# Kernel tuning notes

Measured on AMD Instinct MI355X. Metric: run time of the kernel, lower is better.

Reference implementation:

```python
import jax, jax.numpy as jnp
import numpy as np

# Config matching init_kwargs / input shapes
DIM = 96        # dim == C
NH = 6          # num_heads
KS = 7          # kernel_size (local window)
GW = 4          # group_width for the grouped conv in Hadamard-attn branch
B, D, H, W = 2, 8, 96, 96
HD = DIM // NH          # head dim (dim_qk == dim_v == dim)
SCALE = HD ** -0.5      # qk_scale default: head_dim**-0.5
PAD = KS // 2
EPS = 1e-5


def setup_inputs() -> dict:
    key = jax.random.key(0)
    ks = jax.random.split(key, 10)
    s = 0.02
    return {
        "x": jax.random.normal(ks[0], (B, DIM, D, H, W), jnp.float32),
        # pre-norm LayerNorm params
        "ln_g": jnp.ones((DIM,), jnp.float32),
        "ln_b": jnp.zeros((DIM,), jnp.float32),
        # q,k projection (fused 1x1): out = 2*dim_qk
        "w_qk": s * jax.random.normal(ks[1], (2 * DIM, DIM), jnp.float32),
        "b_qk": jnp.zeros((2 * DIM,), jnp.float32),
        # v projection (1x1)
        "w_v": s * jax.random.normal(ks[2], (DIM, DIM), jnp.float32),
        "b_v": jnp.zeros((DIM,), jnp.float32),
        # Hadamard-attention branch: grouped KSxKS conv (groups = DIM//GW)
        "w_a1": s * jax.random.normal(ks[3], (DIM, GW, KS, KS), jnp.float32),
        "b_a1": jnp.zeros((DIM,), jnp.float32),
        # 1x1 conv producing per-head local attention logits (NH * KS^2 channels)
        "w_a2": s * jax.random.normal(ks[4], (NH * KS * KS, DIM), jnp.float32),
        "b_a2": jnp.zeros((NH * KS * KS,), jnp.float32),
        # ghost head (lam=1, gamma=1): attn = h_attn * ghost_mul + ghost_add
        "g_mul": 1.0 + s * jax.random.normal(ks[5], (NH * KS * KS,), jnp.float32),
        "g_add": s * jax.random.normal(ks[6], (NH * KS * KS,), jnp.float32),
        # output projection (1x1)
        "w_p": s * jax.random.normal(ks[7], (DIM, DIM), jnp.float32),
        "b_p": jnp.zeros((DIM,), jnp.float32),
    }


def _elsa_block(x, ln_g, ln_b, w_qk, b_qk, w_v, b_v, w_a1, b_a1, w_a2, b_a2,
                g_mul, g_add, w_p, b_p):
    """x: (Bp, H, W, C) channel-last frames. Pre-norm residual ELSA attention."""
    Bp, Hh, Ww, C = x.shape
    # LayerNorm over channels
    mu = jnp.mean(x, axis=-1, keepdims=True)
    var = jnp.mean(jnp.square(x - mu), axis=-1, keepdims=True)
    xn = (x - mu) * jax.lax.rsqrt(var + EPS) * ln_g + ln_b

    # 1x1 q,k,v projections (channel-last matmuls)
    qk = xn @ w_qk.T + b_qk                      # (Bp,H,W,2C)
    q, k = jnp.split(qk, 2, axis=-1)
    v = xn @ w_v.T + b_v                         # (Bp,H,W,C)

    # Hadamard product -> attention logits via grouped conv + GELU + 1x1
    h = jnp.transpose(q * k * SCALE, (0, 3, 1, 2))   # (Bp,C,H,W) NCHW
    a = jax.lax.conv_general_dilated(
        h, w_a1, window_strides=(1, 1), padding='SAME',
        feature_group_count=C // GW) + b_a1[None, :, None, None]
    a = jax.nn.gelu(a, approximate=False)
    a = jnp.einsum('bchw,oc->bohw', a, w_a2) + b_a2[None, :, None, None]

    # ghost head (lam=1, gamma=1): elementwise scale + static bias per (head, tap)
    attn = a * g_mul[None, :, None, None] + g_add[None, :, None, None]
    attn = attn.reshape(Bp, NH, KS * KS, Hh, Ww)     # (Bp,nh,k^2,H,W)

    # local window aggregation (unfold-free: 49 shifted fused multiply-adds)
    vr = jnp.transpose(v, (0, 3, 1, 2)).reshape(Bp, NH, HD, Hh, Ww)
    vp = jnp.pad(vr, ((0, 0), (0, 0), (0, 0), (PAD, PAD), (PAD, PAD)))
    out = jnp.zeros_like(vr)
    for i in range(KS):
        for j in range(KS):
            out = out + attn[:, :, i * KS + j, None] * vp[:, :, :, i:i + Hh, j:j + Ww]

    out = jnp.transpose(out.reshape(Bp, C, Hh, Ww), (0, 2, 3, 1))  # (Bp,H,W,C)
    y = out @ w_p.T + b_p
    return x + y


def reference(x, ln_g, ln_b, w_qk, b_qk, w_v, b_v, w_a1, b_a1, w_a2, b_a2,
              g_mul, g_add, w_p, b_p):
    b, c, d, hh, ww = x.shape
    # 'b c s h w -> (b s) h w c'
    xf = jnp.transpose(x, (0, 2, 3, 4, 1)).reshape(b * d, hh, ww, c)
    yf = _elsa_block(xf, ln_g, ln_b, w_qk, b_qk, w_v, b_v, w_a1, b_a1,
                     w_a2, b_a2, g_mul, g_add, w_p, b_p)
    # '(b s) h w c -> b c s h w'
    return jnp.transpose(yf.reshape(b, d, hh, ww, c), (0, 4, 1, 2, 3))
```

## Files before the change

kernel.cpp:

```cpp
#include <hip/hip_runtime.h>
#include <hip/hip_bf16.h>


typedef unsigned short u16;
typedef short bf16x8 __attribute__((ext_vector_type(8)));
typedef float floatx4 __attribute__((ext_vector_type(4)));
typedef unsigned short ushort8 __attribute__((ext_vector_type(8)));
typedef unsigned int uint4v __attribute__((ext_vector_type(4)));
typedef unsigned int uint2v __attribute__((ext_vector_type(2)));
typedef _Float16 f16x2 __attribute__((ext_vector_type(2)));

#define PIX      9216
#define SCALE_QK 0.25f

__device__ __forceinline__ float lo2f(unsigned int u) {
  union { unsigned int i; float f; } z; z.i = u << 16; return z.f;
}
__device__ __forceinline__ float hi2f(unsigned int u) {
  union { unsigned int i; float f; } z; z.i = u & 0xFFFF0000u; return z.f;
}
__device__ __forceinline__ u16 f2b(float f) {
  union { float f; unsigned int i; } z; z.f = f;
  unsigned int r = z.i + 0x7fffu + ((z.i >> 16) & 1u);
  return (u16)(r >> 16);
}
__device__ __forceinline__ u16 f2h(float f) {
  _Float16 h = (_Float16)f;
  union { _Float16 h; u16 u; } z; z.h = h; return z.u;
}
__device__ __forceinline__ f16x2 upk(unsigned int u) {
  union { unsigned int u; f16x2 h; } z; z.u = u; return z.h;
}
__device__ __forceinline__ f16x2 pkfma(unsigned int w, unsigned int x, f16x2 c) {
#if __has_builtin(__builtin_elementwise_fma)
  return __builtin_elementwise_fma(upk(w), upk(x), c);
#else
  return upk(w) * upk(x) + c;
#endif
}

__global__ void k_prep(const float* __restrict__ w_qk, const float* __restrict__ b_qk,
                       const float* __restrict__ w_v,  const float* __restrict__ b_v,
                       const float* __restrict__ w_a1,
                       const float* __restrict__ w_a2, const float* __restrict__ b_a2,
                       const float* __restrict__ g_mul,const float* __restrict__ g_add,
                       const float* __restrict__ w_p,  const float* __restrict__ b_p,
                       u16* __restrict__ W2, float* __restrict__ bias2,
                       u16* __restrict__ WA2, float* __restrict__ biasA2,
                       u16* __restrict__ WP, float* __restrict__ biasP,
                       unsigned int* __restrict__ WCV) {
  int i = blockIdx.x * 256 + threadIdx.x;
  if (i < 30720) {
    int r = i / 96, ci = i % 96;
    float val = 0.f;
    if (r < 192) { int src = (r & 1) ? (96 + (r >> 1)) : (r >> 1); val = w_qk[src * 96 + ci]; }
    else if (r < 288) val = w_v[(r - 192) * 96 + ci];
    W2[i] = f2b(val);
  } else if (i < 31040) {
    int r = i - 30720; float bv = 0.f;
    if (r < 192) { int src = (r & 1) ? (96 + (r >> 1)) : (r >> 1); bv = b_qk[src]; }
    else if (r < 288) bv = b_v[r - 192];
    bias2[r] = bv;
  } else if (i < 61760) {
    int j = i - 31040; int r = j / 96, ci = j % 96;
    float wv = 0.f;
    if (r < 294) wv = w_a2[r * 96 + ci] * g_mul[r];
    WA2[j] = f2b(wv);
  } else if (i < 62080) {
    int r = i - 61760; float bv = 0.f;
    if (r < 294) bv = b_a2[r] * g_mul[r] + g_add[r];
    biasA2[r] = bv;
  } else if (i < 74368) {
    int j = i - 62080; int r = j / 96;
    WP[j] = (r < 96) ? f2b(w_p[j]) : (u16)0;
  } else if (i < 74496) {
    int r = i - 74368;
    biasP[r] = (r < 96) ? b_p[r] : 0.f;
  } else if (i < 93312) {
    int j = i - 74496;
    int kx = j % 7, co = (j / 7) & 3, ky = (j / 28) % 7, ch = (j / 196) & 3, g = j / 784;
    float w = w_a1[(g * 4 + co) * 196 + ch * 49 + ky * 7 + kx];
    unsigned int hw = f2h(w);
    WCV[j] = hw | (hw << 16);
  }
}

template <int MODE>
__global__ __launch_bounds__(256) void k_gemm(const u16* __restrict__ X,
                                              const u16* __restrict__ W,
                                              const float* __restrict__ bias,
                                              u16* __restrict__ out0,
                                              u16* __restrict__ out1,
                                              float* __restrict__ outF,
                                              const float* __restrict__ resid,
                                              const float* __restrict__ lg,
                                              const float* __restrict__ lb,
                                              int fArg) {
  constexpr int NC = (MODE == 2) ? 2 : 5;
  __shared__ u16 lw[64 * 104];
  __shared__ u16 lx[64 * 104];
  const int tid = threadIdx.x;
  const int fc = blockIdx.y;
  const int f = (MODE == 1) ? (fArg + fc) : fc;
  const int p0 = blockIdx.x * 64;

  if constexpr (MODE == 0) {
    const int pix = tid >> 2, sub = tid & 3;
    const int b = f >> 3, d = f & 7;
    const size_t xbase = ((size_t)(b * 768 + d)) * PIX + p0 + pix;
    float xv[24];
    #pragma unroll
    for (int k = 0; k < 24; ++k)
      xv[k] = resid[xbase + (size_t)(sub * 24 + k) * 73728];
    float s = 0.f, ss = 0.f;
    #pragma unroll
    for (int k = 0; k < 24; ++k) { s += xv[k]; ss += xv[k] * xv[k]; }
    s += __shfl_xor(s, 1);  ss += __shfl_xor(ss, 1);
    s += __shfl_xor(s, 2);  ss += __shfl_xor(ss, 2);
    float mu = s * (1.f / 96.f);
    float var = ss * (1.f / 96.f) - mu * mu;
    float rs = rsqrtf(var + 1e-5f);
    unsigned int* dst = (unsigned int*)&lx[pix * 104 + sub * 24];
    #pragma unroll
    for (int k = 0; k < 12; ++k) {
      int c = sub * 24 + 2 * k;
      u16 lo = f2b((xv[2 * k]     - mu) * rs * lg[c]     + lb[c]);
      u16 hi = f2b((xv[2 * k + 1] - mu) * rs * lg[c + 1] + lb[c + 1]);
      dst[k] = (unsigned int)lo | ((unsigned int)hi << 16);
    }
  } else {
    for (int idx = tid; idx < 768; idx += 256) {
      int s2 = idx >> 6, r = idx & 63;
      const u16* src0 = &X[((size_t)(f * 24 + 2 * s2) * PIX + p0 + r) * 4];
      const u16* src1 = &X[((size_t)(f * 24 + 2 * s2 + 1) * PIX + p0 + r) * 4];
      *(uint2v*)&lx[r * 104 + s2 * 8]     = *(const uint2v*)src0;
      *(uint2v*)&lx[r * 104 + s2 * 8 + 4] = *(const uint2v*)src1;
    }
  }
  __syncthreads();

  const int lane = tid & 63, wv = tid >> 6;
  const int cw = (wv >> 1) * 32, pw = (wv & 1) * 32;
  const int m = lane & 15, quad = lane >> 4;

  for (int cot = 0; cot < NC; ++cot) {
    for (int ch = tid; ch < 768; ch += 256) {
      int r = ch / 12, s2 = ch % 12;
      *(uint4v*)&lw[r * 104 + s2 * 8] =
          *(const uint4v*)&W[(size_t)(cot * 64 + r) * 96 + s2 * 8];
    }
    __syncthreads();

    floatx4 acc[2][2] = {};
    for (int ks = 0; ks < 3; ++ks) {
      int ko = ks * 32 + quad * 8;
      bf16x8 a0 = *(const bf16x8*)&lw[(cw + m) * 104 + ko];
      bf16x8 a1 = *(const bf16x8*)&lw[(cw + 16 + m) * 104 + ko];
      bf16x8 b0 = *(const bf16x8*)&lx[(pw + m) * 104 + ko];
      bf16x8 b1 = *(const bf16x8*)&lx[(pw + 16 + m) * 104 + ko];
      acc[0][0] = __builtin_amdgcn_mfma_f32_16x16x32_bf16(a0, b0, acc[0][0], 0, 0, 0);
      acc[0][1] = __builtin_amdgcn_mfma_f32_16x16x32_bf16(a0, b1, acc[0][1], 0, 0, 0);
      acc[1][0] = __builtin_amdgcn_mfma_f32_16x16x32_bf16(a1, b0, acc[1][0], 0, 0, 0);
      acc[1][1] = __builtin_amdgcn_mfma_f32_16x16x32_bf16(a1, b1, acc[1][1], 0, 0, 0);
    }

    for (int mt = 0; mt < 2; ++mt)
      for (int nt = 0; nt < 2; ++nt) {
        int R = cot * 64 + cw + mt * 16 + quad * 4;
        int pc = p0 + pw + nt * 16 + m;
        floatx4 v4 = acc[mt][nt];
        if (MODE == 0) {
          if (cot < 3) {
            float q0 = v4[0] + bias[R + 0], k0 = v4[1] + bias[R + 1];
            float q1 = v4[2] + bias[R + 2], k1 = v4[3] + bias[R + 3];
            int hc = R >> 1;
            out0[((size_t)f * 96 + hc) * PIX + pc]     = f2h(q0 * k0 * SCALE_QK);
            out0[((size_t)f * 96 + hc + 1) * PIX + pc] = f2h(q1 * k1 * SCALE_QK);
          } else {
            for (int r = 0; r < 4; ++r) {
              int vr = R + r - 192;
              if (vr < 96) out1[((size_t)f * 96 + vr) * PIX + pc] = f2b(v4[r] + bias[R + r]);
            }
          }
        } else if (MODE == 1) {
          for (int r = 0; r < 4; ++r) {
            int o = R + r;
            if (o < 294) out0[((size_t)fc * 294 + o) * PIX + pc] = f2b(v4[r] + bias[o]);
          }
        } else {
          int b = f >> 3, dd = f & 7;
          for (int r = 0; r < 4; ++r) {
            int o = R + r;
            if (o < 96) {
              size_t gi = ((size_t)(b * 96 + o) * 8 + dd) * PIX + pc;
              outF[gi] = resid[gi] + v4[r] + bias[o];
            }
          }
        }
      }
    __syncthreads();
  }
}

__global__ __launch_bounds__(256, 4) void k_conv(const u16* __restrict__ h,
                                                 const unsigned int* __restrict__ wcv,
                                                 const float* __restrict__ b_a1,
                                                 u16* __restrict__ a_t) {
  __shared__ u16 li[4 * 22 * 104];
  const int g = blockIdx.x, ty = blockIdx.y, f = blockIdx.z;
  const int tid = threadIdx.x;
  const int gb = g * 4, y0 = ty * 16;
  for (int idx = tid; idx < 4576; idx += 256) {
    int row = idx / 52;
    int jd  = idx - row * 52;
    int ch  = row / 22;
    int rr  = row - ch * 22;
    int ay  = y0 - 3 + rr;
    unsigned int val = 0;
    if (jd >= 2 && jd <= 49 && ay >= 0 && ay < 96)
      val = *(const unsigned int*)&h[((size_t)f * 96 + gb + ch) * PIX + ay * 96 + (2 * jd - 4)];
    *(unsigned int*)&li[row * 104 + 2 * jd] = val;
  }
  __syncthreads();

  const int y = tid >> 4;
  const int x0 = (tid & 15) * 6;
  f16x2 pacc[4][3];
  #pragma unroll
  for (int co = 0; co < 4; ++co)
    #pragma unroll
    for (int p = 0; p < 3; ++p) pacc[co][p] = upk(0u);

  for (int ch = 0; ch < 4; ++ch) {
    const unsigned int* wch = &wcv[784 * g + 196 * ch];
    for (int ky = 0; ky < 7; ++ky) {
      const unsigned int* lsrc =
          (const unsigned int*)&li[(ch * 22 + (y + ky)) * 104 + x0];
      unsigned int D0 = lsrc[0], D1 = lsrc[1], D2 = lsrc[2], D3 = lsrc[3];
      unsigned int D4 = lsrc[4], D5 = lsrc[5], D6 = lsrc[6];
      unsigned int S0 = __builtin_amdgcn_alignbit(D1, D0, 16);
      unsigned int S1 = __builtin_amdgcn_alignbit(D2, D1, 16);
      unsigned int S2 = __builtin_amdgcn_alignbit(D3, D2, 16);
      unsigned int S3 = __builtin_amdgcn_alignbit(D4, D3, 16);
      unsigned int S4 = __builtin_amdgcn_alignbit(D5, D4, 16);
      unsigned int S5 = __builtin_amdgcn_alignbit(D6, D5, 16);
      const unsigned int* wb = wch + 28 * ky;
      #pragma unroll
      for (int co = 0; co < 4; ++co) {
        unsigned int w0 = wb[co * 7 + 0], w1 = wb[co * 7 + 1];
        unsigned int w2 = wb[co * 7 + 2], w3 = wb[co * 7 + 3];
        unsigned int w4 = wb[co * 7 + 4], w5 = wb[co * 7 + 5];
        unsigned int w6 = wb[co * 7 + 6];
        f16x2 a;
        a = pacc[co][0];
        a = pkfma(w0, S0, a); a = pkfma(w1, D1, a); a = pkfma(w2, S1, a);
        a = pkfma(w3, D2, a); a = pkfma(w4, S2, a); a = pkfma(w5, D3, a);
        a = pkfma(w6, S3, a); pacc[co][0] = a;
        a = pacc[co][1];
        a = pkfma(w0, S1, a); a = pkfma(w1, D2, a); a = pkfma(w2, S2, a);
        a = pkfma(w3, D3, a); a = pkfma(w4, S3, a); a = pkfma(w5, D4, a);
        a = pkfma(w6, S4, a); pacc[co][1] = a;
        a = pacc[co][2];
        a = pkfma(w0, S2, a); a = pkfma(w1, D3, a); a = pkfma(w2, S3, a);
        a = pkfma(w3, D4, a); a = pkfma(w4, S4, a); a = pkfma(w5, D5, a);
        a = pkfma(w6, S5, a); pacc[co][2] = a;
      }
    }
  }

  size_t obase = ((size_t)(f * 24 + g) * PIX + (size_t)(y0 + y) * 96 + x0) * 4;
  float bv0 = b_a1[gb + 0], bv1 = b_a1[gb + 1], bv2 = b_a1[gb + 2], bv3 = b_a1[gb + 3];
  #pragma unroll
  for (int p = 0; p < 3; ++p) {
    ushort8 r8;
    #pragma unroll
    for (int co = 0; co < 4; ++co) {
      float bv = (co == 0) ? bv0 : (co == 1) ? bv1 : (co == 2) ? bv2 : bv3;
      f16x2 v = pacc[co][p];
      float a0 = (float)v[0] + bv, a1 = (float)v[1] + bv;
      r8[co]     = f2b(0.5f * a0 * (1.f + erff(a0 * 0.70710678118f)));
      r8[co + 4] = f2b(0.5f * a1 * (1.f + erff(a1 * 0.70710678118f)));
    }
    *(ushort8*)&a_t[obase + p * 8] = r8;
  }
}

__global__ __launch_bounds__(256, 4) void k_aggr(const u16* __restrict__ attn_c,
                                                 const u16* __restrict__ v,
                                                 u16* __restrict__ out_t,
                                                 int fbase) {
  __shared__ u16 lv[4 * 22 * 104];
  const int wgid = blockIdx.x + 24 * (blockIdx.y + 6 * blockIdx.z);
  const int xcd = wgid & 7;
  const int member = (wgid >> 3) & 3;
  const int slot = wgid >> 5;
  const int gidx = slot * 8 + xcd;
  const int cqh = gidx % 6;
  const int ty = (gidx / 6) % 6;
  const int fc = gidx / 36;
  const int cq = cqh * 4 + member;
  const int f = fbase + fc;
  const int tid = threadIdx.x;
  const int c0 = cq * 4, y0 = ty * 16;
  const int head = c0 >> 4;
  for (int idx = tid; idx < 4 * 22 * 104; idx += 256) {
    int col = idx % 104;
    int rr = (idx / 104) % 22;
    int ch = idx / (104 * 22);
    int ax = col - 3, ay = y0 - 3 + rr;
    u16 val = 0;
    if (ax >= 0 && ax < 96 && ay >= 0 && ay < 96)
      val = v[((size_t)f * 96 + c0 + ch) * PIX + ay * 96 + ax];
    lv[idx] = val;
  }
  __syncthreads();

  const int y = tid >> 4;
  const int x0 = (tid & 15) * 6;
  float acc[4][6] = {};
  const int prow = (y0 + y) * 96 + x0;

  for (int i = 0; i < 7; ++i) {
    float vrow[4][12];
    #pragma unroll
    for (int ch = 0; ch < 4; ++ch) {
      const unsigned int* lsrc = (const unsigned int*)&lv[(ch * 22 + (y + i)) * 104 + x0];
      #pragma unroll
      for (int t = 0; t < 6; ++t) {
        unsigned int u = lsrc[t];
        vrow[ch][2 * t]     = lo2f(u);
        vrow[ch][2 * t + 1] = hi2f(u);
      }
    }
    #pragma unroll
    for (int j = 0; j < 7; ++j) {
      const unsigned int* asrc = (const unsigned int*)
          &attn_c[((size_t)fc * 294 + head * 49 + i * 7 + j) * PIX + prow];
      unsigned int u0 = asrc[0], u1 = asrc[1], u2 = asrc[2];
      float av[6] = {lo2f(u0), hi2f(u0), lo2f(u1), hi2f(u1), lo2f(u2), hi2f(u2)};
      #pragma unroll
      for (int o = 0; o < 6; ++o)
        #pragma unroll
        for (int ch = 0; ch < 4; ++ch)
          acc[ch][o] += av[o] * vrow[ch][o + j];
    }
  }

  size_t obase = ((size_t)(f * 24 + cq) * PIX + prow) * 4;
  #pragma unroll
  for (int o = 0; o < 6; o += 2) {
    ushort8 r8;
    #pragma unroll
    for (int ch = 0; ch < 4; ++ch) {
      r8[ch]     = f2b(acc[ch][o]);
      r8[ch + 4] = f2b(acc[ch][o + 1]);
    }
    *(ushort8*)&out_t[obase + o * 4] = r8;
  }
}

extern "C" void kernel_launch(void* const* d_in, const int* in_sizes, int n_in,
                              void* d_out, int out_size, void* d_ws, size_t ws_size,
                              hipStream_t stream) {
  const float* x    = (const float*)d_in[0];
  const float* ln_g = (const float*)d_in[1];
  const float* ln_b = (const float*)d_in[2];
  const float* w_qk = (const float*)d_in[3];
  const float* b_qk = (const float*)d_in[4];
  const float* w_v  = (const float*)d_in[5];
  const float* b_v  = (const float*)d_in[6];
  const float* w_a1 = (const float*)d_in[7];
  const float* b_a1 = (const float*)d_in[8];
  const float* w_a2 = (const float*)d_in[9];
  const float* b_a2 = (const float*)d_in[10];
  const float* g_mul= (const float*)d_in[11];
  const float* g_add= (const float*)d_in[12];
  const float* w_p  = (const float*)d_in[13];
  const float* b_p  = (const float*)d_in[14];

  char* ws = (char*)d_ws;
  u16*   W2    = (u16*)(ws + 0);
  float* bias2 = (float*)(ws + 61440);
  u16*   WA2   = (u16*)(ws + 62720);
  float* biasA2= (float*)(ws + 124160);
  u16*   WP    = (u16*)(ws + 125440);
  float* biasP = (float*)(ws + 150016);
  unsigned int* WCV = (unsigned int*)(ws + 150528);
  u16*   a_t   = (u16*)(ws + 225792);
  u16*   hbuf  = (u16*)(ws + 28537344);
  u16*   vbuf  = (u16*)(ws + 56848896);
  u16*   attnc = (u16*)(ws + 85160448);

  k_prep<<<365, 256, 0, stream>>>(w_qk, b_qk, w_v, b_v, w_a1, w_a2, b_a2, g_mul, g_add,
                                  w_p, b_p, W2, bias2, WA2, biasA2, WP, biasP, WCV);
  k_gemm<0><<<dim3(144, 16), 256, 0, stream>>>(nullptr, W2, bias2, hbuf, vbuf,
                                               nullptr, x, ln_g, ln_b, 0);
  k_conv<<<dim3(24, 6, 16), 256, 0, stream>>>(hbuf, WCV, b_a1, a_t);
  for (int c = 0; c < 2; ++c) {
    k_gemm<1><<<dim3(144, 8), 256, 0, stream>>>(a_t, WA2, biasA2,
                                                attnc, nullptr, nullptr, nullptr,
                                                nullptr, nullptr, c * 8);
    k_aggr<<<dim3(24, 6, 8), 256, 0, stream>>>(attnc, vbuf, hbuf , c * 8);
  }
  k_gemm<2><<<dim3(144, 16), 256, 0, stream>>>(hbuf , WP, biasP,
                                               nullptr, nullptr, (float*)d_out, x,
                                               nullptr, nullptr, 0);
}
```

Before: 378.7 us.

## Switch attention and value tensors to fp16 and use packed-FMA aggregation

The v projection and attention-logit outputs are now stored as fp16 instead of bf16. The local aggregation kernel then accumulates with packed half2 FMAs, and odd and even tap alignments are built with alignbit, so per-element bf16-to-float unpacking is no longer needed. The LDS fill now loads 32-bit pairs instead of 16-bit scalars. This cuts conversion ALU work and halves the number of FMA instructions, but accumulating 49 products in fp16 loses precision and risks overflow compared with fp32.

```diff
diff --git a/kernel.cpp b/kernel.cpp
--- a/kernel.cpp
+++ b/kernel.cpp
@@ -179,13 +179,13 @@
           } else {
             for (int r = 0; r < 4; ++r) {
               int vr = R + r - 192;
-              if (vr < 96) out1[((size_t)f * 96 + vr) * PIX + pc] = f2b(v4[r] + bias[R + r]);
+              if (vr < 96) out1[((size_t)f * 96 + vr) * PIX + pc] = f2h(v4[r] + bias[R + r]);
             }
           }
         } else if (MODE == 1) {
           for (int r = 0; r < 4; ++r) {
             int o = R + r;
-            if (o < 294) out0[((size_t)fc * 294 + o) * PIX + pc] = f2b(v4[r] + bias[o]);
+            if (o < 294) out0[((size_t)fc * 294 + o) * PIX + pc] = f2h(v4[r] + bias[o]);
           }
         } else {
           int b = f >> 3, dd = f & 7;
@@ -303,59 +303,69 @@
   const int tid = threadIdx.x;
   const int c0 = cq * 4, y0 = ty * 16;
   const int head = c0 >> 4;
-  for (int idx = tid; idx < 4 * 22 * 104; idx += 256) {
-    int col = idx % 104;
-    int rr = (idx / 104) % 22;
-    int ch = idx / (104 * 22);
-    int ax = col - 3, ay = y0 - 3 + rr;
-    u16 val = 0;
-    if (ax >= 0 && ax < 96 && ay >= 0 && ay < 96)
-      val = v[((size_t)f * 96 + c0 + ch) * PIX + ay * 96 + ax];
-    lv[idx] = val;
+  for (int idx = tid; idx < 4576; idx += 256) {
+    int row = idx / 52;
+    int jd  = idx - row * 52;
+    int ch  = row / 22;
+    int rr  = row - ch * 22;
+    int ay  = y0 - 3 + rr;
+    unsigned int val = 0;
+    if (jd >= 2 && jd <= 49 && ay >= 0 && ay < 96)
+      val = *(const unsigned int*)&v[((size_t)f * 96 + c0 + ch) * PIX + ay * 96 + (2 * jd - 4)];
+    *(unsigned int*)&lv[row * 104 + 2 * jd] = val;
   }
   __syncthreads();
 
   const int y = tid >> 4;
   const int x0 = (tid & 15) * 6;
-  float acc[4][6] = {};
   const int prow = (y0 + y) * 96 + x0;
+  f16x2 pacc[4][3];
+  #pragma unroll
+  for (int ch = 0; ch < 4; ++ch)
+    #pragma unroll
+    for (int t = 0; t < 3; ++t) pacc[ch][t] = upk(0u);
 
   for (int i = 0; i < 7; ++i) {
-    float vrow[4][12];
+    unsigned int vD[4][7], vS[4][6];
     #pragma unroll
     for (int ch = 0; ch < 4; ++ch) {
       const unsigned int* lsrc = (const unsigned int*)&lv[(ch * 22 + (y + i)) * 104 + x0];
       #pragma unroll
-      for (int t = 0; t < 6; ++t) {
-        unsigned int u = lsrc[t];
-        vrow[ch][2 * t]     = lo2f(u);
-        vrow[ch][2 * t + 1] = hi2f(u);
-      }
+      for (int t = 0; t < 7; ++t) vD[ch][t] = lsrc[t];
+      #pragma unroll
+      for (int t = 0; t < 6; ++t)
+        vS[ch][t] = __builtin_amdgcn_alignbit(vD[ch][t + 1], vD[ch][t], 16);
     }
     #pragma unroll
     for (int j = 0; j < 7; ++j) {
       const unsigned int* asrc = (const unsigned int*)
           &attn_c[((size_t)fc * 294 + head * 49 + i * 7 + j) * PIX + prow];
-      unsigned int u0 = asrc[0], u1 = asrc[1], u2 = asrc[2];
-      float av[6] = {lo2f(u0), hi2f(u0), lo2f(u1), hi2f(u1), lo2f(u2), hi2f(u2)};
+      unsigned int a0 = asrc[0], a1 = asrc[1], a2 = asrc[2];
       #pragma unroll
-      for (int o = 0; o < 6; ++o)
-        #pragma unroll
-        for (int ch = 0; ch < 4; ++ch)
-          acc[ch][o] += av[o] * vrow[ch][o + j];
+      for (int ch = 0; ch < 4; ++ch) {
+        unsigned int p0v, p1v, p2v;
+        if (j & 1) { p0v = vD[ch][(j + 1) / 2];     p1v = vD[ch][1 + (j + 1) / 2];
+                     p2v = vD[ch][2 + (j + 1) / 2]; }
+        else       { p0v = vS[ch][j / 2];           p1v = vS[ch][1 + j / 2];
+                     p2v = vS[ch][2 + j / 2]; }
+        pacc[ch][0] = pkfma(a0, p0v, pacc[ch][0]);
+        pacc[ch][1] = pkfma(a1, p1v, pacc[ch][1]);
+        pacc[ch][2] = pkfma(a2, p2v, pacc[ch][2]);
+      }
     }
   }
 
   size_t obase = ((size_t)(f * 24 + cq) * PIX + prow) * 4;
   #pragma unroll
-  for (int o = 0; o < 6; o += 2) {
+  for (int t = 0; t < 3; ++t) {
     ushort8 r8;
     #pragma unroll
     for (int ch = 0; ch < 4; ++ch) {
-      r8[ch]     = f2b(acc[ch][o]);
-      r8[ch + 4] = f2b(acc[ch][o + 1]);
-    }
-    *(ushort8*)&out_t[obase + o * 4] = r8;
+      f16x2 pv = pacc[ch][t];
+      r8[ch]     = f2b((float)pv[0]);
+      r8[ch + 4] = f2b((float)pv[1]);
+    }
+    *(ushort8*)&out_t[obase + t * 8] = r8;
   }
 }
 
```

Measured after the change: 356.2 us. 5.9% less time.
